# Performance work log

Measured on AMD Instinct MI355X. Metric: run time of the kernel, lower is better.

## Reference

```python
import jax, jax.numpy as jnp
import numpy as np

SYNC = 0.15
DEBATE = 0.15
N_FACTIONS = 8


def faction_sync_debate(h, step):
    # h: [Na, H] hidden rows of alive cells (contiguous, as gathered by alive_idx)
    n, H = h.shape
    n_f = min(N_FACTIONS, n // 2)
    if n_f < 2:
        return h
    fs = n // n_f
    hb = h[: n_f * fs].reshape(n_f, fs, H)
    fm = hb.mean(axis=1, keepdims=True)                  # faction means
    hb = (1.0 - SYNC) * hb + SYNC * fm                   # sync toward faction mean
    if step > 5:                                          # step is a static Python int
        # post-sync faction means equal pre-sync means; global opinion = mean of faction means
        go = hb.mean(axis=1).mean(axis=0)                # [H]
        dc = max(1, fs // 4)
        hb = hb.at[:, :dc].set((1.0 - DEBATE) * hb[:, :dc] + DEBATE * go)
    return jnp.concatenate([hb.reshape(n_f * fs, H), h[n_f * fs:]], axis=0)


def setup_inputs() -> dict:
    key = jax.random.key(0)
    ks = jax.random.split(key, 16)
    n_cells, n_alive = 262144, 131072
    in_d, hid, out_d = 64, 128, 64
    s = 0.1
    alive_idx = jnp.sort(jax.random.permutation(ks[14], n_cells)[:n_alive])
    return {
        "x": jax.random.normal(ks[0], (1, in_d), jnp.float32),
        "hiddens": jax.random.normal(ks[1], (n_cells, hid), jnp.float32) * 0.1,
        "Wa1": jax.random.normal(ks[2], (128, in_d + hid), jnp.float32) * s,
        "ba1": jax.random.normal(ks[3], (128,), jnp.float32) * s,
        "Wa2": jax.random.normal(ks[4], (out_d, 128), jnp.float32) * s,
        "ba2": jax.random.normal(ks[5], (out_d,), jnp.float32) * s,
        "Wg1": jax.random.normal(ks[6], (128, in_d + hid), jnp.float32) * s,
        "bg1": jax.random.normal(ks[7], (128,), jnp.float32) * s,
        "Wg2": jax.random.normal(ks[8], (out_d, 128), jnp.float32) * s,
        "bg2": jax.random.normal(ks[9], (out_d,), jnp.float32) * s,
        "W_ih": jax.random.normal(ks[10], (3 * hid, out_d + 1), jnp.float32) * s,
        "W_hh": jax.random.normal(ks[11], (3 * hid, hid), jnp.float32) * s,
        "b_ih": jax.random.normal(ks[12], (3 * hid,), jnp.float32) * s,
        "b_hh": jax.random.normal(ks[13], (3 * hid,), jnp.float32) * s,
        "alive_idx": alive_idx,
        "step": 10,
    }


def reference(x, hiddens, Wa1, ba1, Wa2, ba2, Wg1, bg1, Wg2, bg2,
              W_ih, W_hh, b_ih, b_hh, alive_idx, step):
    # Gather alive cells and run the tiny MLP+GRU for all of them at once
    h = hiddens[alive_idx]                                # [Na, H]
    xb = jnp.broadcast_to(x, (h.shape[0], x.shape[-1]))   # same x for every cell
    c = jnp.concatenate([xb, h], axis=-1)                 # [Na, in+H]
    a = jax.nn.relu(c @ Wa1.T + ba1) @ Wa2.T + ba2        # engine_a
    g = jax.nn.relu(c @ Wg1.T + bg1) @ Wg2.T + bg2        # engine_g
    out = a - g                                           # [Na, D]
    tension = jnp.mean(out * out, axis=-1, keepdims=True) # [Na, 1]
    # GRUCell (torch gate order r, z, n); mem_input is detached in the original
    mem_in = jax.lax.stop_gradient(jnp.concatenate([out, tension], axis=-1))
    gi = mem_in @ W_ih.T + b_ih                           # [Na, 3H]
    gh = h @ W_hh.T + b_hh                                # [Na, 3H]
    H = h.shape[-1]
    ir, iz, inn = gi[:, :H], gi[:, H:2 * H], gi[:, 2 * H:]
    hr, hz, hn = gh[:, :H], gh[:, H:2 * H], gh[:, 2 * H:]
    r = jax.nn.sigmoid(ir + hr)
    z = jax.nn.sigmoid(iz + hz)
    nn_ = jnp.tanh(inn + r * hn)
    new_h = jax.lax.stop_gradient((1.0 - z) * nn_ + z * h)  # detached in original
    new_h = faction_sync_debate(new_h, step)
    new_hiddens = hiddens.at[alive_idx].set(new_h)        # scatter-back state update
    # tension-softmax-weighted combination (weights detached via .item() in torch)
    t = tension[:, 0]
    w = jax.lax.stop_gradient(jax.nn.softmax(t, axis=0))
    combined = jnp.sum(w[:, None] * out, axis=0, keepdims=True)  # [1, D]
    mean_tension = jnp.mean(jax.lax.stop_gradient(t))
    return combined, mean_tension, new_hiddens
```

## Files before the change

kernel.cpp:

```cpp
#include <hip/hip_runtime.h>
#include <math.h>

#define TMC 64

typedef __attribute__((ext_vector_type(4))) float f32x4;
typedef __attribute__((ext_vector_type(8))) short bf16x8;

#define MFMA16(a,b,c) __builtin_amdgcn_mfma_f32_16x16x32_bf16((a),(b),(c),0,0,0)

__device__ __forceinline__ float sigmoidf_(float x){ return 1.0f/(1.0f + __expf(-x)); }
__device__ __forceinline__ float tanhf_(float x){
  float e = __expf(2.0f*x);
  return 1.0f - 2.0f/(e + 1.0f);
}

__device__ __forceinline__ unsigned short f2bf(float f){
  unsigned u = __float_as_uint(f);
  unsigned r = (u + 0x7FFFu + ((u>>16)&1u)) >> 16;
  return (unsigned short)r;
}
__device__ __forceinline__ unsigned pack2(float a, float b){
  return (unsigned)f2bf(a) | ((unsigned)f2bf(b)<<16);
}
__device__ __forceinline__ float bf2f(unsigned short u){ return __uint_as_float(((unsigned)u)<<16); }

__device__ __forceinline__ bf16x8 lds_ld8(const ushort* base, int byte){
  return *reinterpret_cast<const bf16x8*>(reinterpret_cast<const char*>(base) + byte);
}

__global__ void k_pre(const float* __restrict__ x,
                      const float* __restrict__ Wa1, const float* __restrict__ ba1,
                      const float* __restrict__ Wg1, const float* __restrict__ bg1,
                      const float* __restrict__ ba2, const float* __restrict__ bg2,
                      const float* __restrict__ bih, const float* __restrict__ bhh,
                      float* __restrict__ xab, float* __restrict__ b2d, float* __restrict__ brz){
  __shared__ float sx[64];
  int tid = threadIdx.x;
  if (tid < 64) sx[tid] = x[tid];
  __syncthreads();
  if (tid < 128){
    const float* w = Wa1 + tid*192;
    float s = ba1[tid];
    #pragma unroll
    for (int i=0;i<64;i++) s += w[i]*sx[i];
    xab[tid] = s;
  } else {
    int j = tid-128;
    const float* w = Wg1 + j*192;
    float s = bg1[j];
    #pragma unroll
    for (int i=0;i<64;i++) s += w[i]*sx[i];
    xab[tid] = s;
  }
  if (tid < 64) b2d[tid] = ba2[tid] - bg2[tid];
  brz[tid] = bih[tid] + bhh[tid];
}

__global__ void k_pack(const float* __restrict__ Wa1, const float* __restrict__ Wg1,
                       const float* __restrict__ Wa2, const float* __restrict__ Wg2,
                       const float* __restrict__ Wih, const float* __restrict__ Whh,
                       ushort* __restrict__ W1f, ushort* __restrict__ W2f,
                       ushort* __restrict__ Wgf, ushort* __restrict__ Whf,
                       float* __restrict__ w64){
  int stride = gridDim.x*blockDim.x;
  int t0 = blockIdx.x*blockDim.x + threadIdx.x;
  for (int i=t0; i<256*128; i+=stride){
    int e=i&7, lane=(i>>3)&63, ks=(i>>9)&3, nt=i>>11;
    int r = nt*16 + (lane&15), k = ks*32 + (lane>>4)*8 + e;
    float v = (r<128) ? Wa1[r*192+64+k] : Wg1[(r-128)*192+64+k];
    W1f[i] = f2bf(v);
  }
  for (int i=t0; i<128*128; i+=stride){
    int e=i&7, lane=(i>>3)&63, ks=(i>>9)&3, nt=i>>11;
    int r = nt*16 + (lane&15), k = ks*32 + (lane>>4)*8 + e;
    float v = (r<64) ? Wa2[r*128+k] : Wg2[(r-64)*128+k];
    W2f[i] = f2bf(v);
  }
  for (int i=t0; i<384*64; i+=stride){
    int e=i&7, lane=(i>>3)&63, ks=(i>>9)&1, nt=i>>10;
    int r = nt*16 + (lane&15), k = ks*32 + (lane>>4)*8 + e;
    Wgf[i] = f2bf(Wih[r*65+k]);
  }
  for (int i=t0; i<384*128; i+=stride){
    int e=i&7, lane=(i>>3)&63, ks=(i>>9)&3, nt=i>>11;
    int r = nt*16 + (lane&15), k = ks*32 + (lane>>4)*8 + e;
    Whf[i] = f2bf(Whh[r*128+k]);
  }
  for (int i=t0; i<384; i+=stride) w64[i] = Wih[i*65+64];
}

__global__ void k_mark(const int* __restrict__ alive, int* __restrict__ iflags, int n){
  int i = blockIdx.x*blockDim.x + threadIdx.x;
  if (i < n) iflags[alive[i]] = i + 1;
}

__global__ __launch_bounds__(256,2) void k_main(
    const float* __restrict__ hiddens, const int* __restrict__ alive,
    const ushort* __restrict__ W1f, const ushort* __restrict__ W2f,
    const ushort* __restrict__ Wgf, const ushort* __restrict__ Whf,
    const float* __restrict__ w64,
    const float* __restrict__ xab, const float* __restrict__ b2d,
    const float* __restrict__ brz,
    const float* __restrict__ bih, const float* __restrict__ bhh,
    float* __restrict__ nh, float* __restrict__ facsum,
    float* __restrict__ recs, unsigned* __restrict__ tmax_u, float* __restrict__ tsum,
    int n, int fs, int nffs)
{
  __shared__ ushort sH[64*128];
  __shared__ __align__(16) ushort arena[64*256];
  __shared__ float sTS[4][64];
  __shared__ float sT[64];
  __shared__ float sE[64];
  __shared__ int   sIdx[TMC];

  ushort* sV1  = arena;
  ushort* sMIH = arena;

  int tid = threadIdx.x;
  int lane = tid & 63;
  int w = tid >> 6;
  int l15 = lane & 15;
  int lg  = lane >> 4;

  int base = blockIdx.x * TMC;
  int nvalid = n - base; if (nvalid > TMC) nvalid = TMC;

  if (tid < TMC){
    int t2 = tid < nvalid ? tid : (nvalid-1);
    sIdx[tid] = alive[base + t2];
  }
  __syncthreads();

  {
    int m = tid >> 2, c0 = (tid & 3) * 32;
    const float* src = hiddens + (size_t)sIdx[m]*128 + c0;
    #pragma unroll
    for (int j=0; j<32; j+=8){
      float4 v0 = *(const float4*)(src + j);
      float4 v1 = *(const float4*)(src + j + 4);
      uint4 pk;
      pk.x = pack2(v0.x, v0.y); pk.y = pack2(v0.z, v0.w);
      pk.z = pack2(v1.x, v1.y); pk.w = pack2(v1.z, v1.w);
      int byte = (m*256 + (c0 + j)*2) ^ ((m&7)<<4);
      *reinterpret_cast<uint4*>(reinterpret_cast<char*>(sH) + byte) = pk;
    }
  }
  __syncthreads();

  {
    int c0 = w*64;
    f32x4 acc[4][4];
    #pragma unroll
    for (int tm=0;tm<4;tm++)
      #pragma unroll
      for (int tn=0;tn<4;tn++) acc[tm][tn] = (f32x4)0.f;
    #pragma unroll
    for (int ks=0; ks<4; ks++){
      bf16x8 a[4], b[4];
      #pragma unroll
      for (int tm=0;tm<4;tm++){
        int row = tm*16 + l15;
        a[tm] = lds_ld8(sH, (row*256 + ks*64 + lg*16) ^ ((row&7)<<4));
      }
      #pragma unroll
      for (int tn=0;tn<4;tn++)
        b[tn] = *(const bf16x8*)(W1f + ((((w*4+tn)*4 + ks)*64 + lane)<<3));
      #pragma unroll
      for (int tm=0;tm<4;tm++)
        #pragma unroll
        for (int tn=0;tn<4;tn++)
          acc[tm][tn] = MFMA16(a[tm], b[tn], acc[tm][tn]);
    }
    #pragma unroll
    for (int tn=0;tn<4;tn++){
      int col = c0 + tn*16 + l15;
      float bias = xab[col];
      #pragma unroll
      for (int tm=0;tm<4;tm++){
        #pragma unroll
        for (int r=0;r<4;r++){
          int row = tm*16 + lg*4 + r;
          float v = fmaxf(acc[tm][tn][r] + bias, 0.f);
          int byte = (row*512 + col*2) ^ ((row&7)<<4);
          *(ushort*)((char*)sV1 + byte) = f2bf(v);
        }
      }
    }
  }
  __syncthreads();

  int jo2 = w*16;
  float outv[4][4];
  {
    f32x4 accA[4], accG[4];
    #pragma unroll
    for (int tm=0;tm<4;tm++){ accA[tm]=(f32x4)0.f; accG[tm]=(f32x4)0.f; }
    #pragma unroll
    for (int ks=0; ks<4; ks++){
      bf16x8 aA[4], aG[4], bA, bG;
      #pragma unroll
      for (int tm=0;tm<4;tm++){
        int row = tm*16 + l15;
        aA[tm] = lds_ld8(sV1, (row*512 + ks*64 + lg*16) ^ ((row&7)<<4));
        aG[tm] = lds_ld8(sV1, (row*512 + 256 + ks*64 + lg*16) ^ ((row&7)<<4));
      }
      bA = *(const bf16x8*)(W2f + (((w*4 + ks)*64 + lane)<<3));
      bG = *(const bf16x8*)(W2f + ((((4+w)*4 + ks)*64 + lane)<<3));
      #pragma unroll
      for (int tm=0;tm<4;tm++){
        accA[tm] = MFMA16(aA[tm], bA, accA[tm]);
        accG[tm] = MFMA16(aG[tm], bG, accG[tm]);
      }
    }
    int col = jo2 + l15;
    float bias = b2d[col];
    #pragma unroll
    for (int tm=0;tm<4;tm++)
      #pragma unroll
      for (int r=0;r<4;r++)
        outv[tm][r] = accA[tm][r] - accG[tm][r] + bias;
  }
  __syncthreads();

  {
    int col = jo2 + l15;
    float p[4][4];
    #pragma unroll
    for (int tm=0;tm<4;tm++){
      #pragma unroll
      for (int r=0;r<4;r++){
        int row = tm*16 + lg*4 + r;
        float o = outv[tm][r];
        int byte = (row*128 + col*2) ^ ((row&7)<<4);
        *(ushort*)((char*)sMIH + byte) = f2bf(o);
        p[tm][r] = o*o;
      }
    }
    #pragma unroll
    for (int off=1; off<16; off<<=1)
      #pragma unroll
      for (int tm=0;tm<4;tm++)
        #pragma unroll
        for (int r=0;r<4;r++) p[tm][r] += __shfl_xor(p[tm][r], off);
    if (l15 == 0){
      #pragma unroll
      for (int tm=0;tm<4;tm++)
        #pragma unroll
        for (int r=0;r<4;r++) sTS[w][tm*16 + lg*4 + r] = p[tm][r];
    }
  }
  __syncthreads();

  if (w == 0){
    int row = lane;
    float t = (sTS[0][row] + sTS[1][row] + sTS[2][row] + sTS[3][row]) * (1.0f/64.0f);
    sT[row] = t;
    bool valid = row < nvalid;
    float m2 = valid ? t : -1.f;
    #pragma unroll
    for (int off=1; off<64; off<<=1) m2 = fmaxf(m2, __shfl_xor(m2, off));
    float e  = valid ? __expf(t - m2) : 0.f;
    float st = valid ? t : 0.f;
    float se = e, ss = st;
    #pragma unroll
    for (int off=1; off<64; off<<=1){ se += __shfl_xor(se, off); ss += __shfl_xor(ss, off); }
    sE[row] = e;
    if (lane == 0){
      float* rec = recs + (size_t)blockIdx.x*66;
      rec[0] = m2; rec[1] = se;
      atomicMax(tmax_u, __float_as_uint(m2));
      atomicAdd(tsum, ss);
    }
  }
  __syncthreads();

  {
    float np = 0.f;
    #pragma unroll
    for (int tm=0;tm<4;tm++)
      #pragma unroll
      for (int r=0;r<4;r++)
        np += sE[tm*16 + lg*4 + r] * outv[tm][r];
    np += __shfl_xor(np, 16);
    np += __shfl_xor(np, 32);
    if (lg == 0) recs[(size_t)blockIdx.x*66 + 2 + jo2 + l15] = np;
  }

  int lastrow = nvalid;
  if (base + lastrow > nffs) lastrow = nffs - base;
  int f0 = (fs > 0 && base < nffs) ? base / fs : 0;
  bool onefac = (lastrow <= 0) || ((base + lastrow - 1) / fs == f0);

  {
    int jo3 = w*32;
    int ntb = 2*w;
    f32x4 aR[4][2], aZ[4][2], aN[4][2], aI[4][2];
    #pragma unroll
    for (int tm=0;tm<4;tm++)
      #pragma unroll
      for (int tn=0;tn<2;tn++){
        aR[tm][tn]=(f32x4)0.f; aZ[tm][tn]=(f32x4)0.f;
        aN[tm][tn]=(f32x4)0.f; aI[tm][tn]=(f32x4)0.f;
      }

    #pragma unroll
    for (int ks=0; ks<4; ks++){
      bf16x8 a[4];
      #pragma unroll
      for (int tm=0;tm<4;tm++){
        int row = tm*16 + l15;
        a[tm] = lds_ld8(sH, (row*256 + ks*64 + lg*16) ^ ((row&7)<<4));
      }
      bf16x8 bR[2], bZ[2], bN[2];
      #pragma unroll
      for (int tn=0;tn<2;tn++){
        bR[tn] = *(const bf16x8*)(Whf + ((((     ntb+tn)*4 + ks)*64 + lane)<<3));
        bZ[tn] = *(const bf16x8*)(Whf + ((((8  + ntb+tn)*4 + ks)*64 + lane)<<3));
        bN[tn] = *(const bf16x8*)(Whf + ((((16 + ntb+tn)*4 + ks)*64 + lane)<<3));
      }
      #pragma unroll
      for (int tm=0;tm<4;tm++)
        #pragma unroll
        for (int tn=0;tn<2;tn++){
          aR[tm][tn] = MFMA16(a[tm], bR[tn], aR[tm][tn]);
          aZ[tm][tn] = MFMA16(a[tm], bZ[tn], aZ[tm][tn]);
          aN[tm][tn] = MFMA16(a[tm], bN[tn], aN[tm][tn]);
        }
    }
    #pragma unroll
    for (int ks=0; ks<2; ks++){
      bf16x8 a[4];
      #pragma unroll
      for (int tm=0;tm<4;tm++){
        int row = tm*16 + l15;
        a[tm] = lds_ld8(sMIH, (row*128 + ks*64 + lg*16) ^ ((row&7)<<4));
      }
      bf16x8 bR[2], bZ[2], bI[2];
      #pragma unroll
      for (int tn=0;tn<2;tn++){
        bR[tn] = *(const bf16x8*)(Wgf + ((((     ntb+tn)*2 + ks)*64 + lane)<<3));
        bZ[tn] = *(const bf16x8*)(Wgf + ((((8  + ntb+tn)*2 + ks)*64 + lane)<<3));
        bI[tn] = *(const bf16x8*)(Wgf + ((((16 + ntb+tn)*2 + ks)*64 + lane)<<3));
      }
      #pragma unroll
      for (int tm=0;tm<4;tm++)
        #pragma unroll
        for (int tn=0;tn<2;tn++){
          aR[tm][tn] = MFMA16(a[tm], bR[tn], aR[tm][tn]);
          aZ[tm][tn] = MFMA16(a[tm], bZ[tn], aZ[tm][tn]);
          aI[tm][tn] = MFMA16(a[tm], bI[tn], aI[tm][tn]);
        }
    }

    #pragma unroll
    for (int tn=0;tn<2;tn++){
      int col = jo3 + tn*16 + l15;
      float bR0 = brz[col],      wR = w64[col];
      float bZ0 = brz[128+col],  wZ = w64[128+col];
      float bI0 = bih[256+col],  wI = w64[256+col];
      float bN0 = bhh[256+col];
      float fsum = 0.f;
      #pragma unroll
      for (int tm=0;tm<4;tm++){
        #pragma unroll
        for (int r=0;r<4;r++){
          int row = tm*16 + lg*4 + r;
          float t = sT[row];
          float rr = sigmoidf_(aR[tm][tn][r] + bR0 + t*wR);
          float zz = sigmoidf_(aZ[tm][tn][r] + bZ0 + t*wZ);
          float nnv = tanhf_(aI[tm][tn][r] + bI0 + t*wI + rr*(aN[tm][tn][r] + bN0));
          int hb = (row*256 + col*2) ^ ((row&7)<<4);
          float hv = bf2f(*(const ushort*)((const char*)sH + hb));
          float v = (1.f - zz)*nnv + zz*hv;
          if (row < nvalid) nh[(size_t)sIdx[row]*128 + col] = v;
          if (onefac){
            if (row < lastrow) fsum += v;
          } else if (row < lastrow){
            atomicAdd(&facsum[((base+row)/fs)*128 + col], v);
          }
        }
      }
      if (onefac && lastrow > 0){
        fsum += __shfl_xor(fsum, 16);
        fsum += __shfl_xor(fsum, 32);
        if (lg == 0) atomicAdd(&facsum[f0*128 + col], fsum);
      }
    }
  }
}

__global__ void k_comb1(const float* __restrict__ recs, int nrec,
                        const unsigned* __restrict__ tmax_u,
                        float* __restrict__ num, float* __restrict__ S){
  int tid = threadIdx.x;
  int c = tid & 63, rg = tid >> 6;
  float M = __uint_as_float(*tmax_u);
  float acc = 0.f, sacc = 0.f;
  for (int r = blockIdx.x*4 + rg; r < nrec; r += gridDim.x*4){
    const float* rec = recs + (size_t)r*66;
    float e = __expf(rec[0] - M);
    acc += e * rec[2+c];
    if (c == 0) sacc += e * rec[1];
  }
  __shared__ float sn[4][64];
  __shared__ float ss[4];
  sn[rg][c] = acc;
  if (c == 0) ss[rg] = sacc;
  __syncthreads();
  if (tid < 64) atomicAdd(&num[tid], sn[0][tid]+sn[1][tid]+sn[2][tid]+sn[3][tid]);
  if (tid == 64) atomicAdd(S, ss[0]+ss[1]+ss[2]+ss[3]);
}

__global__ void k_final(const float* __restrict__ num, const float* __restrict__ S,
                        const float* __restrict__ tsum, const float* __restrict__ facsum,
                        float* __restrict__ out, float* __restrict__ go, float* __restrict__ fmn,
                        int n, int n_f, int fs){
  int tid = threadIdx.x;
  if (tid < 64) out[tid] = num[tid] / *S;
  else if (tid == 64) out[64] = *tsum / (float)n;
  if (tid >= 128 && n_f >= 2){
    int j = tid - 128;
    float s = 0.f;
    for (int f=0; f<n_f; f++){
      float v = facsum[f*128+j];
      s += v;
      fmn[f*128+j] = v / (float)fs;
    }
    go[j] = s / (float)(n_f*fs);
  }
}

__global__ void k_post(const float* __restrict__ hid, const int* __restrict__ iflags,
                       const float* __restrict__ fmn, const float* __restrict__ go,
                       const int* __restrict__ step_p,
                       float* __restrict__ nh, int fs, int dc, int nffs, int total){
  bool debate = (*step_p > 5);
  int stride = gridDim.x*blockDim.x;
  for (int idx = blockIdx.x*blockDim.x + threadIdx.x; idx < total; idx += stride){
    int c = idx >> 5, q = idx & 31, j0 = q*4;
    size_t off = (size_t)c*128 + j0;
    int fl = iflags[c];
    if (fl == 0){
      float4 h4 = *(const float4*)(hid + off);
      nh[off] = h4.x; nh[off+1] = h4.y; nh[off+2] = h4.z; nh[off+3] = h4.w;
    } else {
      int i = fl - 1;
      if (i < nffs){
        float v0 = nh[off], v1 = nh[off+1], v2 = nh[off+2], v3 = nh[off+3];
        int f = i / fs;
        float4 fm4 = *(const float4*)(fmn + f*128 + j0);
        v0 = 0.85f*v0 + 0.15f*fm4.x;
        v1 = 0.85f*v1 + 0.15f*fm4.y;
        v2 = 0.85f*v2 + 0.15f*fm4.z;
        v3 = 0.85f*v3 + 0.15f*fm4.w;
        if (debate && (i - f*fs) < dc){
          float4 g4 = *(const float4*)(go + j0);
          v0 = 0.85f*v0 + 0.15f*g4.x;
          v1 = 0.85f*v1 + 0.15f*g4.y;
          v2 = 0.85f*v2 + 0.15f*g4.z;
          v3 = 0.85f*v3 + 0.15f*g4.w;
        }
        nh[off] = v0; nh[off+1] = v1; nh[off+2] = v2; nh[off+3] = v3;
      }
    }
  }
}

extern "C" void kernel_launch(void* const* d_in, const int* in_sizes, int n_in,
                              void* d_out, int out_size, void* d_ws, size_t ws_size,
                              hipStream_t stream){
  const float* x    = (const float*)d_in[0];
  const float* hid  = (const float*)d_in[1];
  const float* Wa1  = (const float*)d_in[2];
  const float* ba1  = (const float*)d_in[3];
  const float* Wa2  = (const float*)d_in[4];
  const float* ba2  = (const float*)d_in[5];
  const float* Wg1  = (const float*)d_in[6];
  const float* bg1  = (const float*)d_in[7];
  const float* Wg2  = (const float*)d_in[8];
  const float* bg2  = (const float*)d_in[9];
  const float* Wih  = (const float*)d_in[10];
  const float* Whh  = (const float*)d_in[11];
  const float* bih  = (const float*)d_in[12];
  const float* bhh  = (const float*)d_in[13];
  const int*   alive= (const int*)d_in[14];
  const int*   step = (const int*)d_in[15];

  int n = in_sizes[14];
  int n_cells = in_sizes[1] / 128;
  int n_f = (n/2 < 8) ? n/2 : 8;
  int fs   = (n_f >= 2) ? n / n_f : 0;
  int nffs = (n_f >= 2) ? n_f * fs : 0;
  int dc   = (fs/4 > 1) ? fs/4 : 1;
  int nblocks = (n + TMC - 1) / TMC;

  float* out = (float*)d_out;
  float* nh  = out + 65;
  float* ws  = (float*)d_ws;

  float* xab   = ws + 0;
  float* b2d   = ws + 256;
  float* brz   = ws + 320;
  float* facs  = ws + 576;
  float* num   = ws + 1600;
  float* Ssum  = ws + 1664;
  float* tsum  = ws + 1665;
  unsigned* tmax_u = (unsigned*)(ws + 1666);
  float* go    = ws + 1668;
  float* fmn   = ws + 1796;
  float* w64   = ws + 2820;
  float* recs  = ws + 3204;
  int recs_end = 3204 + ((nblocks*66 + 3) & ~3);
  int* iflags  = (int*)(ws + recs_end);
  int woff = (recs_end + n_cells + 3) & ~3;
  ushort* W1f  = (ushort*)(ws + woff);
  ushort* W2f  = (ushort*)(ws + woff + 16384);
  ushort* Wgf  = (ushort*)(ws + woff + 24576);
  ushort* Whf  = (ushort*)(ws + woff + 36864);

  hipMemsetAsync(ws + 576, 0, 1092*sizeof(float), stream);
  hipMemsetAsync(iflags, 0, (size_t)n_cells*sizeof(int), stream);

  k_pre<<<1,256,0,stream>>>(x, Wa1, ba1, Wg1, bg1, ba2, bg2, bih, bhh, xab, b2d, brz);
  k_pack<<<256,256,0,stream>>>(Wa1, Wg1, Wa2, Wg2, Wih, Whh, W1f, W2f, Wgf, Whf, w64);
  k_mark<<<(n+255)/256,256,0,stream>>>(alive, iflags, n);
  k_main<<<nblocks,256,0,stream>>>(hid, alive, W1f, W2f, Wgf, Whf, w64, xab, b2d, brz,
                                   bih, bhh, nh, facs, recs, tmax_u, tsum,
                                   n, fs, nffs);
  k_comb1<<<64,256,0,stream>>>(recs, nblocks, tmax_u, num, Ssum);
  k_final<<<1,256,0,stream>>>(num, Ssum, tsum, facs, out, go, fmn, n, n_f, fs);
  k_post<<<2048,256,0,stream>>>(hid, iflags, fmn, go, step, nh, fs, dc, nffs, n_cells*32);
}
```

Measured before the change: 183.4 us.

## Fuse setup kernels, move dead-cell copy into main kernel, shrink post pass

Merges the precompute, weight-pack and alive-marking kernels into one launch. Moves the copy of non-alive hidden rows into the tail of the main kernel, so the post pass only visits alive faction rows through alive_idx instead of sweeping all cells. Also switches bf16 conversion to the hardware packed-convert instruction, raises wave priority around MFMA loops, and hoists tension loads into registers. The aim is fewer launches and less redundant full-array traffic, at the cost of a longer main-kernel tail and uncoalesced gathered accesses in the post pass.

Result: slower. 210.5 us (+14.8%).

```diff
diff --git a/kernel.cpp b/kernel.cpp
--- a/kernel.cpp
+++ b/kernel.cpp
@@ -19,51 +19,57 @@
   unsigned r = (u + 0x7FFFu + ((u>>16)&1u)) >> 16;
   return (unsigned short)r;
 }
-__device__ __forceinline__ unsigned pack2(float a, float b){
-  return (unsigned)f2bf(a) | ((unsigned)f2bf(b)<<16);
-}
 __device__ __forceinline__ float bf2f(unsigned short u){ return __uint_as_float(((unsigned)u)<<16); }
+
+__device__ __forceinline__ unsigned cvt_pk2(float lo, float hi){
+  unsigned r;
+  asm("v_cvt_pk_bf16_f32 %0, %1, %2" : "=v"(r) : "v"(lo), "v"(hi));
+  return r;
+}
+__device__ __forceinline__ unsigned short f2bf_hw(float v){
+  return (unsigned short)cvt_pk2(v, v);
+}
 
 __device__ __forceinline__ bf16x8 lds_ld8(const ushort* base, int byte){
   return *reinterpret_cast<const bf16x8*>(reinterpret_cast<const char*>(base) + byte);
 }
 
-__global__ void k_pre(const float* __restrict__ x,
-                      const float* __restrict__ Wa1, const float* __restrict__ ba1,
-                      const float* __restrict__ Wg1, const float* __restrict__ bg1,
-                      const float* __restrict__ ba2, const float* __restrict__ bg2,
-                      const float* __restrict__ bih, const float* __restrict__ bhh,
-                      float* __restrict__ xab, float* __restrict__ b2d, float* __restrict__ brz){
-  __shared__ float sx[64];
-  int tid = threadIdx.x;
-  if (tid < 64) sx[tid] = x[tid];
-  __syncthreads();
-  if (tid < 128){
-    const float* w = Wa1 + tid*192;
-    float s = ba1[tid];
-    #pragma unroll
-    for (int i=0;i<64;i++) s += w[i]*sx[i];
-    xab[tid] = s;
-  } else {
-    int j = tid-128;
-    const float* w = Wg1 + j*192;
-    float s = bg1[j];
-    #pragma unroll
-    for (int i=0;i<64;i++) s += w[i]*sx[i];
-    xab[tid] = s;
-  }
-  if (tid < 64) b2d[tid] = ba2[tid] - bg2[tid];
-  brz[tid] = bih[tid] + bhh[tid];
-}
-
-__global__ void k_pack(const float* __restrict__ Wa1, const float* __restrict__ Wg1,
+__global__ void k_init(const float* __restrict__ x,
+                       const float* __restrict__ Wa1, const float* __restrict__ ba1,
+                       const float* __restrict__ Wg1, const float* __restrict__ bg1,
                        const float* __restrict__ Wa2, const float* __restrict__ Wg2,
+                       const float* __restrict__ ba2, const float* __restrict__ bg2,
                        const float* __restrict__ Wih, const float* __restrict__ Whh,
+                       const float* __restrict__ bih, const float* __restrict__ bhh,
+                       const int* __restrict__ alive,
+                       float* __restrict__ xab, float* __restrict__ b2d, float* __restrict__ brz,
                        ushort* __restrict__ W1f, ushort* __restrict__ W2f,
                        ushort* __restrict__ Wgf, ushort* __restrict__ Whf,
-                       float* __restrict__ w64){
+                       float* __restrict__ w64, unsigned* __restrict__ iflg, int n){
+  int tid = threadIdx.x;
+  if (blockIdx.x == 0){
+    __shared__ float sx[64];
+    if (tid < 64) sx[tid] = x[tid];
+    __syncthreads();
+    if (tid < 128){
+      const float* w = Wa1 + tid*192;
+      float s = ba1[tid];
+      #pragma unroll
+      for (int i=0;i<64;i++) s += w[i]*sx[i];
+      xab[tid] = s;
+    } else {
+      int j = tid-128;
+      const float* w = Wg1 + j*192;
+      float s = bg1[j];
+      #pragma unroll
+      for (int i=0;i<64;i++) s += w[i]*sx[i];
+      xab[tid] = s;
+    }
+    if (tid < 64) b2d[tid] = ba2[tid] - bg2[tid];
+    brz[tid] = bih[tid] + bhh[tid];
+  }
   int stride = gridDim.x*blockDim.x;
-  int t0 = blockIdx.x*blockDim.x + threadIdx.x;
+  int t0 = blockIdx.x*blockDim.x + tid;
   for (int i=t0; i<256*128; i+=stride){
     int e=i&7, lane=(i>>3)&63, ks=(i>>9)&3, nt=i>>11;
     int r = nt*16 + (lane&15), k = ks*32 + (lane>>4)*8 + e;
@@ -87,11 +93,7 @@
     Whf[i] = f2bf(Whh[r*128+k]);
   }
   for (int i=t0; i<384; i+=stride) w64[i] = Wih[i*65+64];
-}
-
-__global__ void k_mark(const int* __restrict__ alive, int* __restrict__ iflags, int n){
-  int i = blockIdx.x*blockDim.x + threadIdx.x;
-  if (i < n) iflags[alive[i]] = i + 1;
+  for (int i=t0; i<n; i+=stride) iflg[alive[i]] = 1u;
 }
 
 __global__ __launch_bounds__(256,2) void k_main(
@@ -102,9 +104,10 @@
     const float* __restrict__ xab, const float* __restrict__ b2d,
     const float* __restrict__ brz,
     const float* __restrict__ bih, const float* __restrict__ bhh,
+    const unsigned* __restrict__ iflg,
     float* __restrict__ nh, float* __restrict__ facsum,
     float* __restrict__ recs, unsigned* __restrict__ tmax_u, float* __restrict__ tsum,
-    int n, int fs, int nffs)
+    int n, int fs, int nffs, int ncells)
 {
   __shared__ ushort sH[64*128];
   __shared__ __align__(16) ushort arena[64*256];
@@ -125,22 +128,18 @@
   int base = blockIdx.x * TMC;
   int nvalid = n - base; if (nvalid > TMC) nvalid = TMC;
 
-  if (tid < TMC){
-    int t2 = tid < nvalid ? tid : (nvalid-1);
-    sIdx[tid] = alive[base + t2];
-  }
-  __syncthreads();
-
   {
     int m = tid >> 2, c0 = (tid & 3) * 32;
-    const float* src = hiddens + (size_t)sIdx[m]*128 + c0;
+    int idx = alive[base + ((m < nvalid) ? m : (nvalid-1))];
+    if ((tid & 3) == 0) sIdx[m] = idx;
+    const float* src = hiddens + (size_t)idx*128 + c0;
     #pragma unroll
     for (int j=0; j<32; j+=8){
       float4 v0 = *(const float4*)(src + j);
       float4 v1 = *(const float4*)(src + j + 4);
       uint4 pk;
-      pk.x = pack2(v0.x, v0.y); pk.y = pack2(v0.z, v0.w);
-      pk.z = pack2(v1.x, v1.y); pk.w = pack2(v1.z, v1.w);
+      pk.x = cvt_pk2(v0.x, v0.y); pk.y = cvt_pk2(v0.z, v0.w);
+      pk.z = cvt_pk2(v1.x, v1.y); pk.w = cvt_pk2(v1.z, v1.w);
       int byte = (m*256 + (c0 + j)*2) ^ ((m&7)<<4);
       *reinterpret_cast<uint4*>(reinterpret_cast<char*>(sH) + byte) = pk;
     }
@@ -154,6 +153,7 @@
     for (int tm=0;tm<4;tm++)
       #pragma unroll
       for (int tn=0;tn<4;tn++) acc[tm][tn] = (f32x4)0.f;
+    __builtin_amdgcn_s_setprio(1);
     #pragma unroll
     for (int ks=0; ks<4; ks++){
       bf16x8 a[4], b[4];
@@ -171,6 +171,7 @@
         for (int tn=0;tn<4;tn++)
           acc[tm][tn] = MFMA16(a[tm], b[tn], acc[tm][tn]);
     }
+    __builtin_amdgcn_s_setprio(0);
     #pragma unroll
     for (int tn=0;tn<4;tn++){
       int col = c0 + tn*16 + l15;
@@ -182,7 +183,7 @@
           int row = tm*16 + lg*4 + r;
           float v = fmaxf(acc[tm][tn][r] + bias, 0.f);
           int byte = (row*512 + col*2) ^ ((row&7)<<4);
-          *(ushort*)((char*)sV1 + byte) = f2bf(v);
+          *(ushort*)((char*)sV1 + byte) = f2bf_hw(v);
         }
       }
     }
@@ -195,6 +196,7 @@
     f32x4 accA[4], accG[4];
     #pragma unroll
     for (int tm=0;tm<4;tm++){ accA[tm]=(f32x4)0.f; accG[tm]=(f32x4)0.f; }
+    __builtin_amdgcn_s_setprio(1);
     #pragma unroll
     for (int ks=0; ks<4; ks++){
       bf16x8 aA[4], aG[4], bA, bG;
@@ -212,6 +214,7 @@
         accG[tm] = MFMA16(aG[tm], bG, accG[tm]);
       }
     }
+    __builtin_amdgcn_s_setprio(0);
     int col = jo2 + l15;
     float bias = b2d[col];
     #pragma unroll
@@ -232,7 +235,7 @@
         int row = tm*16 + lg*4 + r;
         float o = outv[tm][r];
         int byte = (row*128 + col*2) ^ ((row&7)<<4);
-        *(ushort*)((char*)sMIH + byte) = f2bf(o);
+        *(ushort*)((char*)sMIH + byte) = f2bf_hw(o);
         p[tm][r] = o*o;
       }
     }
@@ -286,6 +289,12 @@
     if (lg == 0) recs[(size_t)blockIdx.x*66 + 2 + jo2 + l15] = np;
   }
 
+  float t16v[4][4];
+  #pragma unroll
+  for (int tm=0;tm<4;tm++)
+    #pragma unroll
+    for (int r=0;r<4;r++) t16v[tm][r] = sT[tm*16 + lg*4 + r];
+
   int lastrow = nvalid;
   if (base + lastrow > nffs) lastrow = nffs - base;
   int f0 = (fs > 0 && base < nffs) ? base / fs : 0;
@@ -303,6 +312,7 @@
         aN[tm][tn]=(f32x4)0.f; aI[tm][tn]=(f32x4)0.f;
       }
 
+    __builtin_amdgcn_s_setprio(1);
     #pragma unroll
     for (int ks=0; ks<4; ks++){
       bf16x8 a[4];
@@ -351,6 +361,7 @@
           aI[tm][tn] = MFMA16(a[tm], bI[tn], aI[tm][tn]);
         }
     }
+    __builtin_amdgcn_s_setprio(0);
 
     #pragma unroll
     for (int tn=0;tn<2;tn++){
@@ -365,7 +376,7 @@
         #pragma unroll
         for (int r=0;r<4;r++){
           int row = tm*16 + lg*4 + r;
-          float t = sT[row];
+          float t = t16v[tm][r];
           float rr = sigmoidf_(aR[tm][tn][r] + bR0 + t*wR);
           float zz = sigmoidf_(aZ[tm][tn][r] + bZ0 + t*wZ);
           float nnv = tanhf_(aI[tm][tn][r] + bI0 + t*wI + rr*(aN[tm][tn][r] + bN0));
@@ -384,6 +395,20 @@
         fsum += __shfl_xor(fsum, 16);
         fsum += __shfl_xor(fsum, 32);
         if (lg == 0) atomicAdd(&facsum[f0*128 + col], fsum);
+      }
+    }
+  }
+
+  {
+    int cpb = (ncells + (int)gridDim.x - 1) / (int)gridDim.x;
+    int c0 = blockIdx.x * cpb;
+    int c1 = c0 + cpb; if (c1 > ncells) c1 = ncells;
+    for (int idx = c0*32 + tid; idx < c1*32; idx += 256){
+      int c = idx >> 5, q = idx & 31, j0 = q*4;
+      if (!iflg[c]){
+        size_t off = (size_t)c*128 + j0;
+        float4 h4 = *(const float4*)(hiddens + off);
+        nh[off] = h4.x; nh[off+1] = h4.y; nh[off+2] = h4.z; nh[off+3] = h4.w;
       }
     }
   }
@@ -430,39 +455,32 @@
   }
 }
 
-__global__ void k_post(const float* __restrict__ hid, const int* __restrict__ iflags,
+__global__ void k_post(const int* __restrict__ alive,
                        const float* __restrict__ fmn, const float* __restrict__ go,
                        const int* __restrict__ step_p,
-                       float* __restrict__ nh, int fs, int dc, int nffs, int total){
+                       float* __restrict__ nh, int fs, int dc, int nffs){
   bool debate = (*step_p > 5);
   int stride = gridDim.x*blockDim.x;
+  int total = nffs*32;
   for (int idx = blockIdx.x*blockDim.x + threadIdx.x; idx < total; idx += stride){
-    int c = idx >> 5, q = idx & 31, j0 = q*4;
-    size_t off = (size_t)c*128 + j0;
-    int fl = iflags[c];
-    if (fl == 0){
-      float4 h4 = *(const float4*)(hid + off);
-      nh[off] = h4.x; nh[off+1] = h4.y; nh[off+2] = h4.z; nh[off+3] = h4.w;
-    } else {
-      int i = fl - 1;
-      if (i < nffs){
-        float v0 = nh[off], v1 = nh[off+1], v2 = nh[off+2], v3 = nh[off+3];
-        int f = i / fs;
-        float4 fm4 = *(const float4*)(fmn + f*128 + j0);
-        v0 = 0.85f*v0 + 0.15f*fm4.x;
-        v1 = 0.85f*v1 + 0.15f*fm4.y;
-        v2 = 0.85f*v2 + 0.15f*fm4.z;
-        v3 = 0.85f*v3 + 0.15f*fm4.w;
-        if (debate && (i - f*fs) < dc){
-          float4 g4 = *(const float4*)(go + j0);
-          v0 = 0.85f*v0 + 0.15f*g4.x;
-          v1 = 0.85f*v1 + 0.15f*g4.y;
-          v2 = 0.85f*v2 + 0.15f*g4.z;
-          v3 = 0.85f*v3 + 0.15f*g4.w;
-        }
-        nh[off] = v0; nh[off+1] = v1; nh[off+2] = v2; nh[off+3] = v3;
-      }
-    }
+    int i = idx >> 5, q = idx & 31, j0 = q*4;
+    int row = alive[i];
+    size_t off = (size_t)row*128 + j0;
+    int f = i / fs;
+    float v0 = nh[off], v1 = nh[off+1], v2 = nh[off+2], v3 = nh[off+3];
+    float4 fm4 = *(const float4*)(fmn + f*128 + j0);
+    v0 = 0.85f*v0 + 0.15f*fm4.x;
+    v1 = 0.85f*v1 + 0.15f*fm4.y;
+    v2 = 0.85f*v2 + 0.15f*fm4.z;
+    v3 = 0.85f*v3 + 0.15f*fm4.w;
+    if (debate && (i - f*fs) < dc){
+      float4 g4 = *(const float4*)(go + j0);
+      v0 = 0.85f*v0 + 0.15f*g4.x;
+      v1 = 0.85f*v1 + 0.15f*g4.y;
+      v2 = 0.85f*v2 + 0.15f*g4.z;
+      v3 = 0.85f*v3 + 0.15f*g4.w;
+    }
+    nh[off] = v0; nh[off+1] = v1; nh[off+2] = v2; nh[off+3] = v3;
   }
 }
 
@@ -511,7 +529,7 @@
   float* w64   = ws + 2820;
   float* recs  = ws + 3204;
   int recs_end = 3204 + ((nblocks*66 + 3) & ~3);
-  int* iflags  = (int*)(ws + recs_end);
+  unsigned* iflags = (unsigned*)(ws + recs_end);
   int woff = (recs_end + n_cells + 3) & ~3;
   ushort* W1f  = (ushort*)(ws + woff);
   ushort* W2f  = (ushort*)(ws + woff + 16384);
@@ -519,15 +537,16 @@
   ushort* Whf  = (ushort*)(ws + woff + 36864);
 
   hipMemsetAsync(ws + 576, 0, 1092*sizeof(float), stream);
-  hipMemsetAsync(iflags, 0, (size_t)n_cells*sizeof(int), stream);
-
-  k_pre<<<1,256,0,stream>>>(x, Wa1, ba1, Wg1, bg1, ba2, bg2, bih, bhh, xab, b2d, brz);
-  k_pack<<<256,256,0,stream>>>(Wa1, Wg1, Wa2, Wg2, Wih, Whh, W1f, W2f, Wgf, Whf, w64);
-  k_mark<<<(n+255)/256,256,0,stream>>>(alive, iflags, n);
+  hipMemsetAsync(iflags, 0, (size_t)n_cells*sizeof(unsigned), stream);
+
+  k_init<<<256,256,0,stream>>>(x, Wa1, ba1, Wg1, bg1, Wa2, Wg2, ba2, bg2,
+                               Wih, Whh, bih, bhh, alive,
+                               xab, b2d, brz, W1f, W2f, Wgf, Whf, w64, iflags, n);
   k_main<<<nblocks,256,0,stream>>>(hid, alive, W1f, W2f, Wgf, Whf, w64, xab, b2d, brz,
-                                   bih, bhh, nh, facs, recs, tmax_u, tsum,
-                                   n, fs, nffs);
+                                   bih, bhh, iflags, nh, facs, recs, tmax_u, tsum,
+                                   n, fs, nffs, n_cells);
   k_comb1<<<64,256,0,stream>>>(recs, nblocks, tmax_u, num, Ssum);
   k_final<<<1,256,0,stream>>>(num, Ssum, tsum, facs, out, go, fmn, n, n_f, fs);
-  k_post<<<2048,256,0,stream>>>(hid, iflags, fmn, go, step, nh, fs, dc, nffs, n_cells*32);
-}
+  if (n_f >= 2)
+    k_post<<<2048,256,0,stream>>>(alive, fmn, go, step, nh, fs, dc, nffs);
+}
```

## Halve main-kernel row tile, raise occupancy, and fuse setup kernels into one

Applied to the files above, without the earlier changes.

Reduces rows per block in the main fused kernel from 64 to 32, which halves shared memory and accumulator registers and raises the launch-bounds occupancy target from 2 to 3 blocks per SIMD. The index gather is folded into the hidden-state load, and the tension values are cached in registers before the GRU epilogue. The three small setup kernels (bias precompute, weight packing, alive-flag marking) are merged into a single launch to cut launch overhead. The cost is twice as many blocks, each re-reading the weight fragments, plus more per-block reduction records and atomics.

Measured after the change: 205.1 us. 1.12x slower.

```diff
diff --git a/kernel.cpp b/kernel.cpp
--- a/kernel.cpp
+++ b/kernel.cpp
@@ -1,7 +1,7 @@
 #include <hip/hip_runtime.h>
 #include <math.h>
 
-#define TMC 64
+#define TMC 32
 
 typedef __attribute__((ext_vector_type(4))) float f32x4;
 typedef __attribute__((ext_vector_type(8))) short bf16x8;
@@ -28,42 +28,42 @@
   return *reinterpret_cast<const bf16x8*>(reinterpret_cast<const char*>(base) + byte);
 }
 
-__global__ void k_pre(const float* __restrict__ x,
-                      const float* __restrict__ Wa1, const float* __restrict__ ba1,
-                      const float* __restrict__ Wg1, const float* __restrict__ bg1,
-                      const float* __restrict__ ba2, const float* __restrict__ bg2,
-                      const float* __restrict__ bih, const float* __restrict__ bhh,
-                      float* __restrict__ xab, float* __restrict__ b2d, float* __restrict__ brz){
-  __shared__ float sx[64];
-  int tid = threadIdx.x;
-  if (tid < 64) sx[tid] = x[tid];
-  __syncthreads();
-  if (tid < 128){
-    const float* w = Wa1 + tid*192;
-    float s = ba1[tid];
-    #pragma unroll
-    for (int i=0;i<64;i++) s += w[i]*sx[i];
-    xab[tid] = s;
-  } else {
-    int j = tid-128;
-    const float* w = Wg1 + j*192;
-    float s = bg1[j];
-    #pragma unroll
-    for (int i=0;i<64;i++) s += w[i]*sx[i];
-    xab[tid] = s;
-  }
-  if (tid < 64) b2d[tid] = ba2[tid] - bg2[tid];
-  brz[tid] = bih[tid] + bhh[tid];
-}
-
-__global__ void k_pack(const float* __restrict__ Wa1, const float* __restrict__ Wg1,
+__global__ void k_init(const float* __restrict__ x,
+                       const float* __restrict__ Wa1, const float* __restrict__ ba1,
+                       const float* __restrict__ Wg1, const float* __restrict__ bg1,
                        const float* __restrict__ Wa2, const float* __restrict__ Wg2,
+                       const float* __restrict__ ba2, const float* __restrict__ bg2,
                        const float* __restrict__ Wih, const float* __restrict__ Whh,
+                       const float* __restrict__ bih, const float* __restrict__ bhh,
+                       const int* __restrict__ alive,
+                       float* __restrict__ xab, float* __restrict__ b2d, float* __restrict__ brz,
                        ushort* __restrict__ W1f, ushort* __restrict__ W2f,
                        ushort* __restrict__ Wgf, ushort* __restrict__ Whf,
-                       float* __restrict__ w64){
+                       float* __restrict__ w64, int* __restrict__ iflg, int n){
+  int tid = threadIdx.x;
+  if (blockIdx.x == 0){
+    __shared__ float sx[64];
+    if (tid < 64) sx[tid] = x[tid];
+    __syncthreads();
+    if (tid < 128){
+      const float* w = Wa1 + tid*192;
+      float s = ba1[tid];
+      #pragma unroll
+      for (int i=0;i<64;i++) s += w[i]*sx[i];
+      xab[tid] = s;
+    } else {
+      int j = tid-128;
+      const float* w = Wg1 + j*192;
+      float s = bg1[j];
+      #pragma unroll
+      for (int i=0;i<64;i++) s += w[i]*sx[i];
+      xab[tid] = s;
+    }
+    if (tid < 64) b2d[tid] = ba2[tid] - bg2[tid];
+    brz[tid] = bih[tid] + bhh[tid];
+  }
   int stride = gridDim.x*blockDim.x;
-  int t0 = blockIdx.x*blockDim.x + threadIdx.x;
+  int t0 = blockIdx.x*blockDim.x + tid;
   for (int i=t0; i<256*128; i+=stride){
     int e=i&7, lane=(i>>3)&63, ks=(i>>9)&3, nt=i>>11;
     int r = nt*16 + (lane&15), k = ks*32 + (lane>>4)*8 + e;
@@ -87,14 +87,10 @@
     Whf[i] = f2bf(Whh[r*128+k]);
   }
   for (int i=t0; i<384; i+=stride) w64[i] = Wih[i*65+64];
-}
-
-__global__ void k_mark(const int* __restrict__ alive, int* __restrict__ iflags, int n){
-  int i = blockIdx.x*blockDim.x + threadIdx.x;
-  if (i < n) iflags[alive[i]] = i + 1;
-}
-
-__global__ __launch_bounds__(256,2) void k_main(
+  for (int i=t0; i<n; i+=stride) iflg[alive[i]] = i + 1;
+}
+
+__global__ __launch_bounds__(256,3) void k_main(
     const float* __restrict__ hiddens, const int* __restrict__ alive,
     const ushort* __restrict__ W1f, const ushort* __restrict__ W2f,
     const ushort* __restrict__ Wgf, const ushort* __restrict__ Whf,
@@ -106,11 +102,11 @@
     float* __restrict__ recs, unsigned* __restrict__ tmax_u, float* __restrict__ tsum,
     int n, int fs, int nffs)
 {
-  __shared__ ushort sH[64*128];
-  __shared__ __align__(16) ushort arena[64*256];
-  __shared__ float sTS[4][64];
-  __shared__ float sT[64];
-  __shared__ float sE[64];
+  __shared__ ushort sH[32*128];
+  __shared__ __align__(16) ushort arena[32*256];
+  __shared__ float sTS[4][32];
+  __shared__ float sT[32];
+  __shared__ float sE[32];
   __shared__ int   sIdx[TMC];
 
   ushort* sV1  = arena;
@@ -125,17 +121,13 @@
   int base = blockIdx.x * TMC;
   int nvalid = n - base; if (nvalid > TMC) nvalid = TMC;
 
-  if (tid < TMC){
-    int t2 = tid < nvalid ? tid : (nvalid-1);
-    sIdx[tid] = alive[base + t2];
-  }
-  __syncthreads();
-
   {
-    int m = tid >> 2, c0 = (tid & 3) * 32;
-    const float* src = hiddens + (size_t)sIdx[m]*128 + c0;
-    #pragma unroll
-    for (int j=0; j<32; j+=8){
+    int m = tid >> 3, c0 = (tid & 7) * 16;
+    int idx = alive[base + ((m < nvalid) ? m : (nvalid-1))];
+    if ((tid & 7) == 0) sIdx[m] = idx;
+    const float* src = hiddens + (size_t)idx*128 + c0;
+    #pragma unroll
+    for (int j=0; j<16; j+=8){
       float4 v0 = *(const float4*)(src + j);
       float4 v1 = *(const float4*)(src + j + 4);
       uint4 pk;
@@ -149,16 +141,16 @@
 
   {
     int c0 = w*64;
-    f32x4 acc[4][4];
-    #pragma unroll
-    for (int tm=0;tm<4;tm++)
+    f32x4 acc[2][4];
+    #pragma unroll
+    for (int tm=0;tm<2;tm++)
       #pragma unroll
       for (int tn=0;tn<4;tn++) acc[tm][tn] = (f32x4)0.f;
     #pragma unroll
     for (int ks=0; ks<4; ks++){
-      bf16x8 a[4], b[4];
-      #pragma unroll
-      for (int tm=0;tm<4;tm++){
+      bf16x8 a[2], b[4];
+      #pragma unroll
+      for (int tm=0;tm<2;tm++){
         int row = tm*16 + l15;
         a[tm] = lds_ld8(sH, (row*256 + ks*64 + lg*16) ^ ((row&7)<<4));
       }
@@ -166,7 +158,7 @@
       for (int tn=0;tn<4;tn++)
         b[tn] = *(const bf16x8*)(W1f + ((((w*4+tn)*4 + ks)*64 + lane)<<3));
       #pragma unroll
-      for (int tm=0;tm<4;tm++)
+      for (int tm=0;tm<2;tm++)
         #pragma unroll
         for (int tn=0;tn<4;tn++)
           acc[tm][tn] = MFMA16(a[tm], b[tn], acc[tm][tn]);
@@ -176,7 +168,7 @@
       int col = c0 + tn*16 + l15;
       float bias = xab[col];
       #pragma unroll
-      for (int tm=0;tm<4;tm++){
+      for (int tm=0;tm<2;tm++){
         #pragma unroll
         for (int r=0;r<4;r++){
           int row = tm*16 + lg*4 + r;
@@ -190,16 +182,16 @@
   __syncthreads();
 
   int jo2 = w*16;
-  float outv[4][4];
+  float outv[2][4];
   {
-    f32x4 accA[4], accG[4];
-    #pragma unroll
-    for (int tm=0;tm<4;tm++){ accA[tm]=(f32x4)0.f; accG[tm]=(f32x4)0.f; }
+    f32x4 accA[2], accG[2];
+    #pragma unroll
+    for (int tm=0;tm<2;tm++){ accA[tm]=(f32x4)0.f; accG[tm]=(f32x4)0.f; }
     #pragma unroll
     for (int ks=0; ks<4; ks++){
-      bf16x8 aA[4], aG[4], bA, bG;
-      #pragma unroll
-      for (int tm=0;tm<4;tm++){
+      bf16x8 aA[2], aG[2], bA, bG;
+      #pragma unroll
+      for (int tm=0;tm<2;tm++){
         int row = tm*16 + l15;
         aA[tm] = lds_ld8(sV1, (row*512 + ks*64 + lg*16) ^ ((row&7)<<4));
         aG[tm] = lds_ld8(sV1, (row*512 + 256 + ks*64 + lg*16) ^ ((row&7)<<4));
@@ -207,7 +199,7 @@
       bA = *(const bf16x8*)(W2f + (((w*4 + ks)*64 + lane)<<3));
       bG = *(const bf16x8*)(W2f + ((((4+w)*4 + ks)*64 + lane)<<3));
       #pragma unroll
-      for (int tm=0;tm<4;tm++){
+      for (int tm=0;tm<2;tm++){
         accA[tm] = MFMA16(aA[tm], bA, accA[tm]);
         accG[tm] = MFMA16(aG[tm], bG, accG[tm]);
       }
@@ -215,7 +207,7 @@
     int col = jo2 + l15;
     float bias = b2d[col];
     #pragma unroll
-    for (int tm=0;tm<4;tm++)
+    for (int tm=0;tm<2;tm++)
       #pragma unroll
       for (int r=0;r<4;r++)
         outv[tm][r] = accA[tm][r] - accG[tm][r] + bias;
@@ -224,9 +216,9 @@
 
   {
     int col = jo2 + l15;
-    float p[4][4];
-    #pragma unroll
-    for (int tm=0;tm<4;tm++){
+    float p[2][4];
+    #pragma unroll
+    for (int tm=0;tm<2;tm++){
       #pragma unroll
       for (int r=0;r<4;r++){
         int row = tm*16 + lg*4 + r;
@@ -239,31 +231,31 @@
     #pragma unroll
     for (int off=1; off<16; off<<=1)
       #pragma unroll
-      for (int tm=0;tm<4;tm++)
+      for (int tm=0;tm<2;tm++)
         #pragma unroll
         for (int r=0;r<4;r++) p[tm][r] += __shfl_xor(p[tm][r], off);
     if (l15 == 0){
       #pragma unroll
-      for (int tm=0;tm<4;tm++)
+      for (int tm=0;tm<2;tm++)
         #pragma unroll
         for (int r=0;r<4;r++) sTS[w][tm*16 + lg*4 + r] = p[tm][r];
     }
   }
   __syncthreads();
 
-  if (w == 0){
+  if (w == 0 && lane < 32){
     int row = lane;
     float t = (sTS[0][row] + sTS[1][row] + sTS[2][row] + sTS[3][row]) * (1.0f/64.0f);
     sT[row] = t;
     bool valid = row < nvalid;
     float m2 = valid ? t : -1.f;
     #pragma unroll
-    for (int off=1; off<64; off<<=1) m2 = fmaxf(m2, __shfl_xor(m2, off));
+    for (int off=1; off<32; off<<=1) m2 = fmaxf(m2, __shfl_xor(m2, off));
     float e  = valid ? __expf(t - m2) : 0.f;
     float st = valid ? t : 0.f;
     float se = e, ss = st;
     #pragma unroll
-    for (int off=1; off<64; off<<=1){ se += __shfl_xor(se, off); ss += __shfl_xor(ss, off); }
+    for (int off=1; off<32; off<<=1){ se += __shfl_xor(se, off); ss += __shfl_xor(ss, off); }
     sE[row] = e;
     if (lane == 0){
       float* rec = recs + (size_t)blockIdx.x*66;
@@ -277,7 +269,7 @@
   {
     float np = 0.f;
     #pragma unroll
-    for (int tm=0;tm<4;tm++)
+    for (int tm=0;tm<2;tm++)
       #pragma unroll
       for (int r=0;r<4;r++)
         np += sE[tm*16 + lg*4 + r] * outv[tm][r];
@@ -286,6 +278,12 @@
     if (lg == 0) recs[(size_t)blockIdx.x*66 + 2 + jo2 + l15] = np;
   }
 
+  float t16v[2][4];
+  #pragma unroll
+  for (int tm=0;tm<2;tm++)
+    #pragma unroll
+    for (int r=0;r<4;r++) t16v[tm][r] = sT[tm*16 + lg*4 + r];
+
   int lastrow = nvalid;
   if (base + lastrow > nffs) lastrow = nffs - base;
   int f0 = (fs > 0 && base < nffs) ? base / fs : 0;
@@ -294,9 +292,9 @@
   {
     int jo3 = w*32;
     int ntb = 2*w;
-    f32x4 aR[4][2], aZ[4][2], aN[4][2], aI[4][2];
-    #pragma unroll
-    for (int tm=0;tm<4;tm++)
+    f32x4 aR[2][2], aZ[2][2], aN[2][2], aI[2][2];
+    #pragma unroll
+    for (int tm=0;tm<2;tm++)
       #pragma unroll
       for (int tn=0;tn<2;tn++){
         aR[tm][tn]=(f32x4)0.f; aZ[tm][tn]=(f32x4)0.f;
@@ -305,9 +303,9 @@
 
     #pragma unroll
     for (int ks=0; ks<4; ks++){
-      bf16x8 a[4];
-      #pragma unroll
-      for (int tm=0;tm<4;tm++){
+      bf16x8 a[2];
+      #pragma unroll
+      for (int tm=0;tm<2;tm++){
         int row = tm*16 + l15;
         a[tm] = lds_ld8(sH, (row*256 + ks*64 + lg*16) ^ ((row&7)<<4));
       }
@@ -319,7 +317,7 @@
         bN[tn] = *(const bf16x8*)(Whf + ((((16 + ntb+tn)*4 + ks)*64 + lane)<<3));
       }
       #pragma unroll
-      for (int tm=0;tm<4;tm++)
+      for (int tm=0;tm<2;tm++)
         #pragma unroll
         for (int tn=0;tn<2;tn++){
           aR[tm][tn] = MFMA16(a[tm], bR[tn], aR[tm][tn]);
@@ -329,9 +327,9 @@
     }
     #pragma unroll
     for (int ks=0; ks<2; ks++){
-      bf16x8 a[4];
-      #pragma unroll
-      for (int tm=0;tm<4;tm++){
+      bf16x8 a[2];
+      #pragma unroll
+      for (int tm=0;tm<2;tm++){
         int row = tm*16 + l15;
         a[tm] = lds_ld8(sMIH, (row*128 + ks*64 + lg*16) ^ ((row&7)<<4));
       }
@@ -343,7 +341,7 @@
         bI[tn] = *(const bf16x8*)(Wgf + ((((16 + ntb+tn)*2 + ks)*64 + lane)<<3));
       }
       #pragma unroll
-      for (int tm=0;tm<4;tm++)
+      for (int tm=0;tm<2;tm++)
         #pragma unroll
         for (int tn=0;tn<2;tn++){
           aR[tm][tn] = MFMA16(a[tm], bR[tn], aR[tm][tn]);
@@ -361,11 +359,11 @@
       float bN0 = bhh[256+col];
       float fsum = 0.f;
       #pragma unroll
-      for (int tm=0;tm<4;tm++){
+      for (int tm=0;tm<2;tm++){
         #pragma unroll
         for (int r=0;r<4;r++){
           int row = tm*16 + lg*4 + r;
-          float t = sT[row];
+          float t = t16v[tm][r];
           float rr = sigmoidf_(aR[tm][tn][r] + bR0 + t*wR);
           float zz = sigmoidf_(aZ[tm][tn][r] + bZ0 + t*wZ);
           float nnv = tanhf_(aI[tm][tn][r] + bI0 + t*wI + rr*(aN[tm][tn][r] + bN0));
@@ -521,9 +519,9 @@
   hipMemsetAsync(ws + 576, 0, 1092*sizeof(float), stream);
   hipMemsetAsync(iflags, 0, (size_t)n_cells*sizeof(int), stream);
 
-  k_pre<<<1,256,0,stream>>>(x, Wa1, ba1, Wg1, bg1, ba2, bg2, bih, bhh, xab, b2d, brz);
-  k_pack<<<256,256,0,stream>>>(Wa1, Wg1, Wa2, Wg2, Wih, Whh, W1f, W2f, Wgf, Whf, w64);
-  k_mark<<<(n+255)/256,256,0,stream>>>(alive, iflags, n);
+  k_init<<<256,256,0,stream>>>(x, Wa1, ba1, Wg1, bg1, Wa2, Wg2, ba2, bg2,
+                               Wih, Whh, bih, bhh, alive,
+                               xab, b2d, brz, W1f, W2f, Wgf, Whf, w64, iflags, n);
   k_main<<<nblocks,256,0,stream>>>(hid, alive, W1f, W2f, Wgf, Whf, w64, xab, b2d, brz,
                                    bih, bhh, nh, facs, recs, tmax_u, tsum,
                                    n, fs, nffs);
```
